# Kernel tuning notes

Measured on AMD Instinct MI355X. Metric: run time of the kernel, lower is better.

Reference implementation:

```python
import jax, jax.numpy as jnp
import numpy as np

V, D, L, H, S = 32000, 512, 4, 8, 2048
HD = D // H
EPS = 1e-5

def setup_inputs() -> dict:
    key = jax.random.key(0)
    ks = jax.random.split(key, 20)
    std = 0.02
    inp = {
        'input_ids': jax.random.randint(ks[0], (2, S), 0, V),
        'tok_emb': jax.random.normal(ks[1], (V, D), jnp.float32) * std,
        'pos_emb': jax.random.normal(ks[2], (S, D), jnp.float32) * std,
        'ln1_w': jnp.ones((L, D), jnp.float32),
        'ln1_b': jnp.zeros((L, D), jnp.float32),
        'qkv_w': jax.random.normal(ks[3], (L, D, 3 * D), jnp.float32) * std,
        'qkv_b': jnp.zeros((L, 3 * D), jnp.float32),
        'proj_w': jax.random.normal(ks[4], (L, D, D), jnp.float32) * std,
        'proj_b': jnp.zeros((L, D), jnp.float32),
        'ln2_w': jnp.ones((L, D), jnp.float32),
        'ln2_b': jnp.zeros((L, D), jnp.float32),
        'fc1_w': jax.random.normal(ks[5], (L, D, 4 * D), jnp.float32) * std,
        'fc1_b': jnp.zeros((L, 4 * D), jnp.float32),
        'fc2_w': jax.random.normal(ks[6], (L, 4 * D, D), jnp.float32) * std,
        'fc2_b': jnp.zeros((L, D), jnp.float32),
        'lnf_w': jnp.ones((D,), jnp.float32),
        'lnf_b': jnp.zeros((D,), jnp.float32),
    }
    return inp

def _layernorm(x, w, b):
    mu = jnp.mean(x, axis=-1, keepdims=True)
    var = jnp.mean(jnp.square(x - mu), axis=-1, keepdims=True)
    return (x - mu) * jax.lax.rsqrt(var + EPS) * w + b

def _attn(x, qkv_w, qkv_b, proj_w, proj_b):
    B, T, C = x.shape
    qkv = x @ qkv_w + qkv_b                       # [B,T,3D]
    q, k, v = jnp.split(qkv, 3, axis=-1)
    q = q.reshape(B, T, H, HD)
    k = k.reshape(B, T, H, HD)
    v = v.reshape(B, T, H, HD)
    att = jnp.einsum('bthd,bshd->bhts', q, k) / jnp.sqrt(jnp.float32(HD))
    causal = jnp.tril(jnp.ones((T, T), bool))
    att = jnp.where(causal, att, -jnp.inf)
    att = jax.nn.softmax(att, axis=-1)
    y = jnp.einsum('bhts,bshd->bthd', att, v).reshape(B, T, C)
    return y @ proj_w + proj_b

def reference(input_ids, tok_emb, pos_emb, ln1_w, ln1_b, qkv_w, qkv_b,
              proj_w, proj_b, ln2_w, ln2_b, fc1_w, fc1_b, fc2_w, fc2_b,
              lnf_w, lnf_b):
    B, T = input_ids.shape
    x = tok_emb[input_ids] + pos_emb[:T]          # [B,T,D]
    for i in range(L):
        h = _layernorm(x, ln1_w[i], ln1_b[i])
        x = x + _attn(h, qkv_w[i], qkv_b[i], proj_w[i], proj_b[i])
        h = _layernorm(x, ln2_w[i], ln2_b[i])
        h = jax.nn.gelu(h @ fc1_w[i] + fc1_b[i], approximate=False)
        x = x + (h @ fc2_w[i] + fc2_b[i])
    x = _layernorm(x, lnf_w, lnf_b)
    return x @ tok_emb.T                          # tied head -> [B,T,V]
```

## Files before the change

kernel.cpp:

```cpp
#include <hip/hip_runtime.h>
#include <math.h>

#define V_SZ 32000
#define D_SZ 512
#define NL 4
#define NH 8
#define SEQ 2048
#define HD 64
#define NB 2
#define M_ROWS (NB * SEQ)

typedef __attribute__((ext_vector_type(8))) short bf16x8;
typedef __attribute__((ext_vector_type(4))) float f32x4;
typedef __attribute__((ext_vector_type(4))) unsigned short u16x4;

__device__ __forceinline__ unsigned short f2bf(float f) {
    unsigned int x = __float_as_uint(f);
    unsigned int r = (x + 0x7FFFu + ((x >> 16) & 1u)) >> 16;
    return (unsigned short)r;
}

__device__ __forceinline__ float gelu_f(float x) {
    return 0.5f * x * (1.0f + erff(x * 0.70710678118654752f));
}

__device__ __forceinline__ void gload16(const void* g, void* l) {
    __builtin_amdgcn_global_load_lds(
        (const __attribute__((address_space(1))) void*)g,
        (__attribute__((address_space(3))) void*)l, 16, 0, 0);
}

__global__ __launch_bounds__(256) void embed_kernel(
    const int* __restrict__ ids, const float* __restrict__ tok,
    const float* __restrict__ pos, float* __restrict__ x) {
    int idx = blockIdx.x * 256 + threadIdx.x;
    int row = idx >> 9;
    int d = idx & 511;
    int t = row & (SEQ - 1);
    x[idx] = tok[(size_t)ids[row] * D_SZ + d] + pos[(size_t)t * D_SZ + d];
}

__global__ __launch_bounds__(256) void ln_kernel(
    const float* __restrict__ x, const float* __restrict__ w,
    const float* __restrict__ b, unsigned short* __restrict__ out) {
    int row = blockIdx.x * 4 + (threadIdx.x >> 6);
    int lane = threadIdx.x & 63;
    const float* xr = x + (size_t)row * D_SZ + lane * 8;
    float4 v0 = *(const float4*)xr;
    float4 v1 = *(const float4*)(xr + 4);
    float s = ((v0.x + v0.y) + (v0.z + v0.w)) + ((v1.x + v1.y) + (v1.z + v1.w));
    #pragma unroll
    for (int off = 1; off < 64; off <<= 1) s += __shfl_xor(s, off);
    float mu = s * (1.0f / 512.0f);
    float d0 = v0.x - mu, d1 = v0.y - mu, d2 = v0.z - mu, d3 = v0.w - mu;
    float d4 = v1.x - mu, d5 = v1.y - mu, d6 = v1.z - mu, d7 = v1.w - mu;
    float q = ((d0 * d0 + d1 * d1) + (d2 * d2 + d3 * d3)) +
              ((d4 * d4 + d5 * d5) + (d6 * d6 + d7 * d7));
    #pragma unroll
    for (int off = 1; off < 64; off <<= 1) q += __shfl_xor(q, off);
    float rs = rsqrtf(q * (1.0f / 512.0f) + 1e-5f);
    const float* wp = w + lane * 8;
    const float* bp = b + lane * 8;
    float4 w0 = *(const float4*)wp, w1 = *(const float4*)(wp + 4);
    float4 b0 = *(const float4*)bp, b1 = *(const float4*)(bp + 4);
    uint4 pk;
    pk.x = (unsigned)f2bf(d0 * rs * w0.x + b0.x) | ((unsigned)f2bf(d1 * rs * w0.y + b0.y) << 16);
    pk.y = (unsigned)f2bf(d2 * rs * w0.z + b0.z) | ((unsigned)f2bf(d3 * rs * w0.w + b0.w) << 16);
    pk.z = (unsigned)f2bf(d4 * rs * w1.x + b1.x) | ((unsigned)f2bf(d5 * rs * w1.y + b1.y) << 16);
    pk.w = (unsigned)f2bf(d6 * rs * w1.z + b1.z) | ((unsigned)f2bf(d7 * rs * w1.w + b1.w) << 16);
    *(uint4*)(out + (size_t)row * D_SZ + lane * 8) = pk;
}

__global__ __launch_bounds__(256) void tconv_kernel(
    const float* __restrict__ in, unsigned short* __restrict__ out, int K, int N) {
    __shared__ float t[32][33];
    int l = blockIdx.z;
    in += (size_t)l * K * N;
    out += (size_t)l * N * K;
    int n0 = blockIdx.x * 32, k0 = blockIdx.y * 32;
    int tx = threadIdx.x & 31, ty = threadIdx.x >> 5;
    #pragma unroll
    for (int p = 0; p < 4; p++) {
        int k = ty + p * 8;
        t[k][tx] = in[(size_t)(k0 + k) * N + n0 + tx];
    }
    __syncthreads();
    #pragma unroll
    for (int p = 0; p < 4; p++) {
        int n = ty + p * 8;
        out[(size_t)(n0 + n) * K + k0 + tx] = f2bf(t[tx][n]);
    }
}

__global__ __launch_bounds__(256) void conv_kernel(
    const float* __restrict__ in, unsigned short* __restrict__ out) {
    int i = blockIdx.x * 256 + threadIdx.x;
    float4 v = ((const float4*)in)[i];
    u16x4 u;
    u.x = f2bf(v.x); u.y = f2bf(v.y); u.z = f2bf(v.z); u.w = f2bf(v.w);
    __builtin_nontemporal_store(u, (u16x4*)out + i);
}

__global__ __launch_bounds__(256) void mattn_kernel(
    const unsigned short* __restrict__ qkv, unsigned short* __restrict__ att) {
    __shared__ unsigned short Ks[64][72];
    __shared__ unsigned short Vt[64][72];
    __shared__ unsigned short Ps[4][16][72];
    int id = blockIdx.x;
    int bh = id >> 5;
    int jraw = id & 31;
    int jt = (id < 256) ? jraw : (31 - jraw);
    int b = bh >> 3, h = bh & 7;
    int tid = threadIdx.x, lane = tid & 63, wid = tid >> 6;
    int q15 = lane & 15, g = lane >> 4;
    int qglob = jt * 64 + wid * 16 + q15;
    const unsigned short* base = qkv + (size_t)b * SEQ * (3 * D_SZ);
    const unsigned short* qptr = base + (size_t)qglob * (3 * D_SZ) + h * HD;
    bf16x8 qf0 = *(const bf16x8*)(qptr + g * 8);
    bf16x8 qf1 = *(const bf16x8*)(qptr + 32 + g * 8);
    #pragma unroll
    for (int i = 0; i < 8; i++) {
        qf0[i] = (short)f2bf(
            __uint_as_float(((unsigned)(unsigned short)qf0[i]) << 16) * 0.125f);
        qf1[i] = (short)f2bf(
            __uint_as_float(((unsigned)(unsigned short)qf1[i]) << 16) * 0.125f);
    }

    f32x4 OT[4];
    f32x4 zero = {0.0f, 0.0f, 0.0f, 0.0f};
    #pragma unroll
    for (int n = 0; n < 4; n++) OT[n] = zero;
    float mrun = -1e30f, lrun = 0.0f;

    int krow = tid >> 3, kprt = tid & 7;
    const unsigned short* kbase = base + D_SZ + h * HD + kprt * 8;
    const unsigned short* vbase = base + 2 * D_SZ + h * HD + kprt * 8;
    bf16x8 kp0, kp1, vp0, vp1;

    kp0 = *(const bf16x8*)(kbase + (size_t)krow * (3 * D_SZ));
    kp1 = *(const bf16x8*)(kbase + (size_t)(32 + krow) * (3 * D_SZ));
    vp0 = *(const bf16x8*)(vbase + (size_t)(2 * krow) * (3 * D_SZ));
    vp1 = *(const bf16x8*)(vbase + (size_t)(2 * krow + 1) * (3 * D_SZ));

    int nt = jt + 1;
    for (int st = 0; st < nt; st++) {
        int s0 = st * 64;
        __syncthreads();
        *(bf16x8*)&Ks[krow][kprt * 8] = kp0;
        *(bf16x8*)&Ks[32 + krow][kprt * 8] = kp1;
        {
            int col = (((krow >> 2) ^ kprt) << 3) | ((2 * krow) & 7);
            #pragma unroll
            for (int i = 0; i < 8; i++) {
                int d = kprt * 8 + i;
                unsigned w = (unsigned)(unsigned short)vp0[i]
                           | ((unsigned)(unsigned short)vp1[i] << 16);
                *(unsigned*)&Vt[d][col] = w;
            }
        }
        __syncthreads();
        if (st + 1 < nt) {
            int s1 = s0 + 64;
            kp0 = *(const bf16x8*)(kbase + (size_t)(s1 + krow) * (3 * D_SZ));
            kp1 = *(const bf16x8*)(kbase + (size_t)(s1 + 32 + krow) * (3 * D_SZ));
            vp0 = *(const bf16x8*)(vbase + (size_t)(s1 + 2 * krow) * (3 * D_SZ));
            vp1 = *(const bf16x8*)(vbase + (size_t)(s1 + 2 * krow + 1) * (3 * D_SZ));
        }

        f32x4 S[4];
        #pragma unroll
        for (int n = 0; n < 4; n++) S[n] = zero;
        #pragma unroll
        for (int n = 0; n < 4; n++)
            S[n] = __builtin_amdgcn_mfma_f32_16x16x32_bf16(
                *(const bf16x8*)&Ks[n * 16 + q15][g * 8], qf0, S[n], 0, 0, 0);
        #pragma unroll
        for (int n = 0; n < 4; n++)
            S[n] = __builtin_amdgcn_mfma_f32_16x16x32_bf16(
                *(const bf16x8*)&Ks[n * 16 + q15][32 + g * 8], qf1, S[n], 0, 0, 0);

        bool diag = (st == jt);
        float sm[4][4];
        float mloc = -1e30f;
        #pragma unroll
        for (int n = 0; n < 4; n++)
            #pragma unroll
            for (int r = 0; r < 4; r++) {
                float s = S[n][r];
                if (diag && (s0 + n * 16 + g * 4 + r) > qglob) s = -1e30f;
                sm[n][r] = s;
                mloc = fmaxf(mloc, s);
            }
        mloc = fmaxf(mloc, __shfl_xor(mloc, 16));
        mloc = fmaxf(mloc, __shfl_xor(mloc, 32));
        float mnew = fmaxf(mrun, mloc);
        float corr = __expf(mrun - mnew);
        lrun *= corr;
        #pragma unroll
        for (int n = 0; n < 4; n++) OT[n] *= corr;
        float lsum = 0.0f;
        #pragma unroll
        for (int n = 0; n < 4; n++) {
            float p0 = __expf(sm[n][0] - mnew);
            float p1 = __expf(sm[n][1] - mnew);
            float p2 = __expf(sm[n][2] - mnew);
            float p3 = __expf(sm[n][3] - mnew);
            lsum += (p0 + p1) + (p2 + p3);
            uint2 pk;
            pk.x = (unsigned)f2bf(p0) | ((unsigned)f2bf(p1) << 16);
            pk.y = (unsigned)f2bf(p2) | ((unsigned)f2bf(p3) << 16);
            *(uint2*)&Ps[wid][q15][n * 16 + g * 4] = pk;
        }
        lsum += __shfl_xor(lsum, 16);
        lsum += __shfl_xor(lsum, 32);
        lrun += lsum;
        mrun = mnew;

        #pragma unroll
        for (int ks = 0; ks < 2; ks++) {
            bf16x8 bp = *(const bf16x8*)&Ps[wid][q15][ks * 32 + g * 8];
            #pragma unroll
            for (int n = 0; n < 4; n++) {
                int d = n * 16 + q15;
                int col = (((ks * 4 + g) ^ ((d >> 3) & 7)) << 3);
                OT[n] = __builtin_amdgcn_mfma_f32_16x16x32_bf16(
                    *(const bf16x8*)&Vt[d][col], bp, OT[n], 0, 0, 0);
            }
        }
    }

    float inv = 1.0f / lrun;
    unsigned short* orow = att + ((size_t)(b * SEQ) + qglob) * D_SZ + h * HD;
    #pragma unroll
    for (int n = 0; n < 4; n++) {
        uint2 u;
        u.x = (unsigned)f2bf(OT[n][0] * inv) | ((unsigned)f2bf(OT[n][1] * inv) << 16);
        u.y = (unsigned)f2bf(OT[n][2] * inv) | ((unsigned)f2bf(OT[n][3] * inv) << 16);
        *(uint2*)(orow + n * 16 + g * 4) = u;
    }
}

template <int BM, int BN, int BK, int WC, bool BIAS, bool GELU_, bool RESID,
          bool OUTBF, bool SWAPXY, bool NTC>
__global__ __launch_bounds__(256) void mgemm_kernel(
    const unsigned short* __restrict__ A,
    const unsigned short* __restrict__ Bt,
    const float* __restrict__ bias,
    const float* __restrict__ resid,
    void* __restrict__ Cv, int M, int N, int K) {
    constexpr int WR = 4 / WC;
    constexpr int WRM = BM / WR;
    constexpr int WCN = BN / WC;
    constexpr int FM = WRM / 16;
    constexpr int FN = WCN / 16;
    constexpr int CPR = BK / 8;
    constexpr int LA = BM * CPR / 256;
    constexpr int LB = BN * CPR / 256;
    __shared__ __attribute__((aligned(16))) unsigned short As[2][BM][BK];
    __shared__ __attribute__((aligned(16))) unsigned short Bs[2][BN][BK];
    int tid = threadIdx.x;
    int lane = tid & 63;
    int wid = tid >> 6;
    int wr = wid / WC, wc = wid % WC;
    int m0 = (SWAPXY ? blockIdx.x : blockIdx.y) * BM;
    int n0 = (SWAPXY ? blockIdx.y : blockIdx.x) * BN;
    int r16 = lane & 15, kg = lane >> 4;

    f32x4 acc[FM][FN];
    f32x4 zero = {0.0f, 0.0f, 0.0f, 0.0f};
    #pragma unroll
    for (int m = 0; m < FM; m++)
        #pragma unroll
        for (int n = 0; n < FN; n++) acc[m][n] = zero;

    const unsigned short* Abase = A + (size_t)m0 * K;
    const unsigned short* Bbase = Bt + (size_t)n0 * K;

    #pragma unroll
    for (int i = 0; i < LA; i++) {
        int c = i * 256 + tid;
        gload16(Abase + (size_t)(c / CPR) * K + (c % CPR) * 8,
                &As[0][c / CPR][(c % CPR) * 8]);
    }
    #pragma unroll
    for (int i = 0; i < LB; i++) {
        int c = i * 256 + tid;
        gload16(Bbase + (size_t)(c / CPR) * K + (c % CPR) * 8,
                &Bs[0][c / CPR][(c % CPR) * 8]);
    }
    __syncthreads();

    unsigned short* a_cur = &As[0][0][0];
    unsigned short* a_nxt = &As[1][0][0];
    unsigned short* b_cur = &Bs[0][0][0];
    unsigned short* b_nxt = &Bs[1][0][0];

    for (int k0 = 0; k0 < K; k0 += BK) {
        if (k0 + BK < K) {
            #pragma unroll
            for (int i = 0; i < LA; i++) {
                int c = i * 256 + tid;
                gload16(Abase + (size_t)(c / CPR) * K + (k0 + BK) + (c % CPR) * 8,
                        a_nxt + c * 8);
            }
            #pragma unroll
            for (int i = 0; i < LB; i++) {
                int c = i * 256 + tid;
                gload16(Bbase + (size_t)(c / CPR) * K + (k0 + BK) + (c % CPR) * 8,
                        b_nxt + c * 8);
            }
        }
        #pragma unroll
        for (int kk = 0; kk < BK / 32; kk++) {
            bf16x8 af[FM], bfr[FN];
            #pragma unroll
            for (int m = 0; m < FM; m++)
                af[m] = *(const bf16x8*)&a_cur[(wr * WRM + m * 16 + r16) * BK +
                                               kk * 32 + kg * 8];
            #pragma unroll
            for (int n = 0; n < FN; n++)
                bfr[n] = *(const bf16x8*)&b_cur[(wc * WCN + n * 16 + r16) * BK +
                                                kk * 32 + kg * 8];
            #pragma unroll
            for (int m = 0; m < FM; m++)
                #pragma unroll
                for (int n = 0; n < FN; n++)
                    acc[m][n] = __builtin_amdgcn_mfma_f32_16x16x32_bf16(
                        af[m], bfr[n], acc[m][n], 0, 0, 0);
        }
        __syncthreads();
        unsigned short* t;
        t = a_cur; a_cur = a_nxt; a_nxt = t;
        t = b_cur; b_cur = b_nxt; b_nxt = t;
    }

    float bvv[FN];
    #pragma unroll
    for (int n = 0; n < FN; n++)
        bvv[n] = BIAS ? bias[n0 + wc * WCN + n * 16 + r16] : 0.0f;
    #pragma unroll
    for (int m = 0; m < FM; m++) {
        int rb = m0 + wr * WRM + m * 16 + kg * 4;
        #pragma unroll
        for (int r = 0; r < 4; r++) {
            size_t rowoff = (size_t)(rb + r) * N;
            #pragma unroll
            for (int n = 0; n < FN; n++) {
                int col = n0 + wc * WCN + n * 16 + r16;
                float v = acc[m][n][r] + bvv[n];
                if (GELU_) v = gelu_f(v);
                if (RESID) v += resid[rowoff + col];
                if (OUTBF) {
                    ((unsigned short*)Cv)[rowoff + col] = f2bf(v);
                } else if (NTC) {
                    __builtin_nontemporal_store(v, (float*)Cv + rowoff + col);
                } else {
                    ((float*)Cv)[rowoff + col] = v;
                }
            }
        }
    }
}

extern "C" void kernel_launch(void* const* d_in, const int* in_sizes, int n_in,
                              void* d_out, int out_size, void* d_ws, size_t ws_size,
                              hipStream_t stream) {
    const int*   ids   = (const int*)d_in[0];
    const float* tok   = (const float*)d_in[1];
    const float* pos   = (const float*)d_in[2];
    const float* ln1w  = (const float*)d_in[3];
    const float* ln1b  = (const float*)d_in[4];
    const float* qkvw  = (const float*)d_in[5];
    const float* qkvb  = (const float*)d_in[6];
    const float* projw = (const float*)d_in[7];
    const float* projb = (const float*)d_in[8];
    const float* ln2w  = (const float*)d_in[9];
    const float* ln2b  = (const float*)d_in[10];
    const float* fc1w  = (const float*)d_in[11];
    const float* fc1b  = (const float*)d_in[12];
    const float* fc2w  = (const float*)d_in[13];
    const float* fc2b  = (const float*)d_in[14];
    const float* lnfw  = (const float*)d_in[15];
    const float* lnfb  = (const float*)d_in[16];
    float* out = (float*)d_out;

    float* x = (float*)d_ws;
    unsigned short* hb = (unsigned short*)(x + (size_t)M_ROWS * D_SZ);
    unsigned short* wq = hb + (size_t)M_ROWS * D_SZ;
    unsigned short* wp = wq + (size_t)NL * D_SZ * 3 * D_SZ;
    unsigned short* w1 = wp + (size_t)NL * D_SZ * D_SZ;
    unsigned short* w2 = w1 + (size_t)NL * D_SZ * 4 * D_SZ;
    unsigned short* qkvb_a = w2 + (size_t)NL * 4 * D_SZ * D_SZ;
    unsigned short* attb = qkvb_a + (size_t)M_ROWS * 3 * D_SZ;
    unsigned short* ffnb = attb + (size_t)M_ROWS * D_SZ;
    unsigned short* tokb = qkvb_a;

    tconv_kernel<<<dim3(1536/32, 512/32, NL), 256, 0, stream>>>(qkvw, wq, D_SZ, 3*D_SZ);
    tconv_kernel<<<dim3(512/32, 512/32, NL), 256, 0, stream>>>(projw, wp, D_SZ, D_SZ);
    tconv_kernel<<<dim3(2048/32, 512/32, NL), 256, 0, stream>>>(fc1w, w1, D_SZ, 4*D_SZ);
    tconv_kernel<<<dim3(512/32, 2048/32, NL), 256, 0, stream>>>(fc2w, w2, 4*D_SZ, D_SZ);

    embed_kernel<<<M_ROWS * D_SZ / 256, 256, 0, stream>>>(ids, tok, pos, x);

    for (int l = 0; l < NL; l++) {
        ln_kernel<<<M_ROWS / 4, 256, 0, stream>>>(x, ln1w + l * D_SZ, ln1b + l * D_SZ, hb);
        mgemm_kernel<64, 128, 64, 2, true, false, false, true, false, false>
            <<<dim3(3 * D_SZ / 128, M_ROWS / 64), 256, 0, stream>>>(
                hb, wq + (size_t)l * 3 * D_SZ * D_SZ, qkvb + (size_t)l * 3 * D_SZ,
                nullptr, qkvb_a, M_ROWS, 3 * D_SZ, D_SZ);
        mattn_kernel<<<(SEQ / 64) * NB * NH, 256, 0, stream>>>(qkvb_a, attb);
        mgemm_kernel<64, 64, 64, 2, true, false, true, false, false, false>
            <<<dim3(D_SZ / 64, M_ROWS / 64), 256, 0, stream>>>(
                attb, wp + (size_t)l * D_SZ * D_SZ, projb + (size_t)l * D_SZ,
                x, x, M_ROWS, D_SZ, D_SZ);
        ln_kernel<<<M_ROWS / 4, 256, 0, stream>>>(x, ln2w + l * D_SZ, ln2b + l * D_SZ, hb);
        mgemm_kernel<64, 128, 64, 2, true, true, false, true, false, false>
            <<<dim3(4 * D_SZ / 128, M_ROWS / 64), 256, 0, stream>>>(
                hb, w1 + (size_t)l * 4 * D_SZ * D_SZ, fc1b + (size_t)l * 4 * D_SZ,
                nullptr, ffnb, M_ROWS, 4 * D_SZ, D_SZ);
        mgemm_kernel<64, 64, 64, 2, true, false, true, false, false, false>
            <<<dim3(D_SZ / 64, M_ROWS / 64), 256, 0, stream>>>(
                ffnb, w2 + (size_t)l * D_SZ * 4 * D_SZ, fc2b + (size_t)l * D_SZ,
                x, x, M_ROWS, D_SZ, 4 * D_SZ);
    }

    ln_kernel<<<M_ROWS / 4, 256, 0, stream>>>(x, lnfw, lnfb, hb);
    conv_kernel<<<V_SZ * D_SZ / 4 / 256, 256, 0, stream>>>(tok, tokb);
    mgemm_kernel<128, 128, 32, 2, false, false, false, false, true, true>
        <<<dim3(M_ROWS / 128, V_SZ / 128), 256, 0, stream>>>(
            hb, tokb, nullptr, nullptr, out, M_ROWS, V_SZ, D_SZ);
}
```

Baseline: 701.7 us.

## Merge prep launches, fuse final LN with tok conversion, stage head epilogue

Folds the four weight transpose-convert launches and the embedding into one prep kernel, and merges the final layernorm with the token-embedding bf16 conversion into one launch, cutting launch count and idle tails. It also rewrites the vocab-head GEMM epilogue to stage accumulators through shared memory, so each thread writes contiguous 64-byte rows with nontemporal stores instead of scattered scalar stores. The bf16 token table buffer moves to the weight region, since the weights are dead by then. The risk is extra syncs and LDS traffic in the epilogue, plus branchy heterogeneous blocks in the fused kernels.

```diff
diff --git a/kernel.cpp b/kernel.cpp
--- a/kernel.cpp
+++ b/kernel.cpp
@@ -30,14 +30,60 @@
         (__attribute__((address_space(3))) void*)l, 16, 0, 0);
 }
 
-__global__ __launch_bounds__(256) void embed_kernel(
+__device__ __forceinline__ void tconv_body(
+    const float* __restrict__ in, unsigned short* __restrict__ out,
+    int K, int N, int lin, float (*t)[33]) {
+    int nx = N / 32, ny = K / 32;
+    int bx = lin % nx;
+    int r2 = lin / nx;
+    int by = r2 % ny;
+    int l = r2 / ny;
+    in += (size_t)l * K * N;
+    out += (size_t)l * N * K;
+    int n0 = bx * 32, k0 = by * 32;
+    int tx = threadIdx.x & 31, ty = threadIdx.x >> 5;
+    #pragma unroll
+    for (int p = 0; p < 4; p++) {
+        int k = ty + p * 8;
+        t[k][tx] = in[(size_t)(k0 + k) * N + n0 + tx];
+    }
+    __syncthreads();
+    #pragma unroll
+    for (int p = 0; p < 4; p++) {
+        int n = ty + p * 8;
+        out[(size_t)(n0 + n) * K + k0 + tx] = f2bf(t[tx][n]);
+    }
+}
+
+#define TCQ 3072
+#define TCP 1024
+#define TC1 4096
+#define TC2 4096
+#define EMB 8192
+
+__global__ __launch_bounds__(256) void prep_kernel(
+    const float* __restrict__ qkvw, const float* __restrict__ projw,
+    const float* __restrict__ fc1w, const float* __restrict__ fc2w,
     const int* __restrict__ ids, const float* __restrict__ tok,
-    const float* __restrict__ pos, float* __restrict__ x) {
-    int idx = blockIdx.x * 256 + threadIdx.x;
+    const float* __restrict__ pos,
+    unsigned short* __restrict__ wq, unsigned short* __restrict__ wp,
+    unsigned short* __restrict__ w1, unsigned short* __restrict__ w2,
+    float* __restrict__ x) {
+    __shared__ float t[32][33];
+    int b = blockIdx.x;
+    if (b < TCQ) { tconv_body(qkvw, wq, D_SZ, 3 * D_SZ, b, t); return; }
+    b -= TCQ;
+    if (b < TCP) { tconv_body(projw, wp, D_SZ, D_SZ, b, t); return; }
+    b -= TCP;
+    if (b < TC1) { tconv_body(fc1w, w1, D_SZ, 4 * D_SZ, b, t); return; }
+    b -= TC1;
+    if (b < TC2) { tconv_body(fc2w, w2, 4 * D_SZ, D_SZ, b, t); return; }
+    b -= TC2;
+    int idx = b * 256 + threadIdx.x;
     int row = idx >> 9;
     int d = idx & 511;
-    int t = row & (SEQ - 1);
-    x[idx] = tok[(size_t)ids[row] * D_SZ + d] + pos[(size_t)t * D_SZ + d];
+    int tt = row & (SEQ - 1);
+    x[idx] = tok[(size_t)ids[row] * D_SZ + d] + pos[(size_t)tt * D_SZ + d];
 }
 
 __global__ __launch_bounds__(256) void ln_kernel(
@@ -71,34 +117,45 @@
     *(uint4*)(out + (size_t)row * D_SZ + lane * 8) = pk;
 }
 
-__global__ __launch_bounds__(256) void tconv_kernel(
-    const float* __restrict__ in, unsigned short* __restrict__ out, int K, int N) {
-    __shared__ float t[32][33];
-    int l = blockIdx.z;
-    in += (size_t)l * K * N;
-    out += (size_t)l * N * K;
-    int n0 = blockIdx.x * 32, k0 = blockIdx.y * 32;
-    int tx = threadIdx.x & 31, ty = threadIdx.x >> 5;
-    #pragma unroll
-    for (int p = 0; p < 4; p++) {
-        int k = ty + p * 8;
-        t[k][tx] = in[(size_t)(k0 + k) * N + n0 + tx];
-    }
-    __syncthreads();
-    #pragma unroll
-    for (int p = 0; p < 4; p++) {
-        int n = ty + p * 8;
-        out[(size_t)(n0 + n) * K + k0 + tx] = f2bf(t[tx][n]);
-    }
-}
-
-__global__ __launch_bounds__(256) void conv_kernel(
-    const float* __restrict__ in, unsigned short* __restrict__ out) {
-    int i = blockIdx.x * 256 + threadIdx.x;
-    float4 v = ((const float4*)in)[i];
-    u16x4 u;
-    u.x = f2bf(v.x); u.y = f2bf(v.y); u.z = f2bf(v.z); u.w = f2bf(v.w);
-    __builtin_nontemporal_store(u, (u16x4*)out + i);
+__global__ __launch_bounds__(256) void lnconv_kernel(
+    const float* __restrict__ x, const float* __restrict__ w,
+    const float* __restrict__ b, unsigned short* __restrict__ out,
+    const float* __restrict__ tok, unsigned short* __restrict__ tokb) {
+    int blk = blockIdx.x;
+    if (blk < M_ROWS / 4) {
+        int row = blk * 4 + (threadIdx.x >> 6);
+        int lane = threadIdx.x & 63;
+        const float* xr = x + (size_t)row * D_SZ + lane * 8;
+        float4 v0 = *(const float4*)xr;
+        float4 v1 = *(const float4*)(xr + 4);
+        float s = ((v0.x + v0.y) + (v0.z + v0.w)) + ((v1.x + v1.y) + (v1.z + v1.w));
+        #pragma unroll
+        for (int off = 1; off < 64; off <<= 1) s += __shfl_xor(s, off);
+        float mu = s * (1.0f / 512.0f);
+        float d0 = v0.x - mu, d1 = v0.y - mu, d2 = v0.z - mu, d3 = v0.w - mu;
+        float d4 = v1.x - mu, d5 = v1.y - mu, d6 = v1.z - mu, d7 = v1.w - mu;
+        float q = ((d0 * d0 + d1 * d1) + (d2 * d2 + d3 * d3)) +
+                  ((d4 * d4 + d5 * d5) + (d6 * d6 + d7 * d7));
+        #pragma unroll
+        for (int off = 1; off < 64; off <<= 1) q += __shfl_xor(q, off);
+        float rs = rsqrtf(q * (1.0f / 512.0f) + 1e-5f);
+        const float* wp = w + lane * 8;
+        const float* bp = b + lane * 8;
+        float4 w0 = *(const float4*)wp, w1 = *(const float4*)(wp + 4);
+        float4 b0 = *(const float4*)bp, b1 = *(const float4*)(bp + 4);
+        uint4 pk;
+        pk.x = (unsigned)f2bf(d0 * rs * w0.x + b0.x) | ((unsigned)f2bf(d1 * rs * w0.y + b0.y) << 16);
+        pk.y = (unsigned)f2bf(d2 * rs * w0.z + b0.z) | ((unsigned)f2bf(d3 * rs * w0.w + b0.w) << 16);
+        pk.z = (unsigned)f2bf(d4 * rs * w1.x + b1.x) | ((unsigned)f2bf(d5 * rs * w1.y + b1.y) << 16);
+        pk.w = (unsigned)f2bf(d6 * rs * w1.z + b1.z) | ((unsigned)f2bf(d7 * rs * w1.w + b1.w) << 16);
+        *(uint4*)(out + (size_t)row * D_SZ + lane * 8) = pk;
+    } else {
+        int i = (blk - M_ROWS / 4) * 256 + threadIdx.x;
+        float4 v = ((const float4*)tok)[i];
+        u16x4 u;
+        u.x = f2bf(v.x); u.y = f2bf(v.y); u.z = f2bf(v.z); u.w = f2bf(v.w);
+        __builtin_nontemporal_store(u, (u16x4*)tokb + i);
+    }
 }
 
 __global__ __launch_bounds__(256) void mattn_kernel(
@@ -256,6 +313,8 @@
     constexpr int CPR = BK / 8;
     constexpr int LA = BM * CPR / 256;
     constexpr int LB = BN * CPR / 256;
+    static_assert(!NTC || (BM == 128 && BN == 128 && BK == 32 && WC == 2),
+                  "NTC transpose-epilogue assumes the head config");
     __shared__ __attribute__((aligned(16))) unsigned short As[2][BM][BK];
     __shared__ __attribute__((aligned(16))) unsigned short Bs[2][BN][BK];
     int tid = threadIdx.x;
@@ -334,6 +393,36 @@
         t = b_cur; b_cur = b_nxt; b_nxt = t;
     }
 
+    if constexpr (NTC) {
+        float* fbuf = (float*)&As[0][0][0];
+        #pragma unroll
+        for (int c = 0; c < 4; c++) {
+            if (wr == (c >> 1)) {
+                #pragma unroll
+                for (int mm = 0; mm < 2; mm++) {
+                    int m = 2 * (c & 1) + mm;
+                    #pragma unroll
+                    for (int n = 0; n < FN; n++)
+                        #pragma unroll
+                        for (int r = 0; r < 4; r++)
+                            fbuf[(mm * 16 + kg * 4 + r) * 128 +
+                                 wc * 64 + n * 16 + r16] = acc[m][n][r];
+                }
+            }
+            __syncthreads();
+            int lrow = tid >> 3;
+            int lcol = (tid & 7) * 16;
+            float* op = (float*)Cv + (size_t)(m0 + c * 32 + lrow) * N + n0 + lcol;
+            #pragma unroll
+            for (int q = 0; q < 4; q++) {
+                f32x4 vv = *(const f32x4*)&fbuf[lrow * 128 + lcol + q * 4];
+                __builtin_nontemporal_store(vv, (f32x4*)(op + q * 4));
+            }
+            __syncthreads();
+        }
+        return;
+    }
+
     float bvv[FN];
     #pragma unroll
     for (int n = 0; n < FN; n++)
@@ -352,8 +441,6 @@
                 if (RESID) v += resid[rowoff + col];
                 if (OUTBF) {
                     ((unsigned short*)Cv)[rowoff + col] = f2bf(v);
-                } else if (NTC) {
-                    __builtin_nontemporal_store(v, (float*)Cv + rowoff + col);
                 } else {
                     ((float*)Cv)[rowoff + col] = v;
                 }
@@ -393,14 +480,10 @@
     unsigned short* qkvb_a = w2 + (size_t)NL * 4 * D_SZ * D_SZ;
     unsigned short* attb = qkvb_a + (size_t)M_ROWS * 3 * D_SZ;
     unsigned short* ffnb = attb + (size_t)M_ROWS * D_SZ;
-    unsigned short* tokb = qkvb_a;
-
-    tconv_kernel<<<dim3(1536/32, 512/32, NL), 256, 0, stream>>>(qkvw, wq, D_SZ, 3*D_SZ);
-    tconv_kernel<<<dim3(512/32, 512/32, NL), 256, 0, stream>>>(projw, wp, D_SZ, D_SZ);
-    tconv_kernel<<<dim3(2048/32, 512/32, NL), 256, 0, stream>>>(fc1w, w1, D_SZ, 4*D_SZ);
-    tconv_kernel<<<dim3(512/32, 2048/32, NL), 256, 0, stream>>>(fc2w, w2, 4*D_SZ, D_SZ);
-
-    embed_kernel<<<M_ROWS * D_SZ / 256, 256, 0, stream>>>(ids, tok, pos, x);
+    unsigned short* tokb = wq;
+
+    prep_kernel<<<TCQ + TCP + TC1 + TC2 + EMB, 256, 0, stream>>>(
+        qkvw, projw, fc1w, fc2w, ids, tok, pos, wq, wp, w1, w2, x);
 
     for (int l = 0; l < NL; l++) {
         ln_kernel<<<M_ROWS / 4, 256, 0, stream>>>(x, ln1w + l * D_SZ, ln1b + l * D_SZ, hb);
@@ -424,8 +507,8 @@
                 x, x, M_ROWS, D_SZ, 4 * D_SZ);
     }
 
-    ln_kernel<<<M_ROWS / 4, 256, 0, stream>>>(x, lnfw, lnfb, hb);
-    conv_kernel<<<V_SZ * D_SZ / 4 / 256, 256, 0, stream>>>(tok, tokb);
+    lnconv_kernel<<<M_ROWS / 4 + V_SZ * D_SZ / 4 / 256, 256, 0, stream>>>(
+        x, lnfw, lnfb, hb, tok, tokb);
     mgemm_kernel<128, 128, 32, 2, false, false, false, false, true, true>
         <<<dim3(M_ROWS / 128, V_SZ / 128), 256, 0, stream>>>(
             hb, tokb, nullptr, nullptr, out, M_ROWS, V_SZ, D_SZ);
```

After: 1.400 ms. 99.6% more time.
